# Kernel optimization log

Hardware: AMD Instinct MI355X
Metric: run time of the kernel (lower is better)

The kernel has to match this reference:

```python
import jax, jax.numpy as jnp
import numpy as np

B, C, N, R = 4, 256, 4096, 8
CR = C // R  # 32


def _bn(x, s, b):
    # inference-mode BatchNorm1d folded to per-channel scale/bias; x: [B, C', N]
    return x * s[:, None] + b[:, None]


def setup_inputs() -> dict:
    key = jax.random.key(0)
    ks = jax.random.split(key, 16)
    sc = 1.0 / np.sqrt(C)
    d = {}
    d["x"] = jax.random.normal(ks[0], (B, C, N), jnp.float32)
    d["qk_w"] = jax.random.normal(ks[1], (CR, C), jnp.float32) * sc  # shared q/k 1x1 conv weight
    d["v_w"] = jax.random.normal(ks[2], (C, C), jnp.float32) * sc
    d["v_b"] = jax.random.normal(ks[3], (C,), jnp.float32) * 0.01
    d["trans_w"] = jax.random.normal(ks[4], (C, C), jnp.float32) * sc
    d["trans_b"] = jax.random.normal(ks[5], (C,), jnp.float32) * 0.01
    d["bn1_s"] = 1.0 + 0.1 * jax.random.normal(ks[6], (CR,), jnp.float32)
    d["bn1_b"] = 0.01 * jax.random.normal(ks[7], (CR,), jnp.float32)
    d["bn2_s"] = 1.0 + 0.1 * jax.random.normal(ks[8], (CR,), jnp.float32)
    d["bn2_b"] = 0.01 * jax.random.normal(ks[9], (CR,), jnp.float32)
    d["bn3_s"] = 1.0 + 0.1 * jax.random.normal(ks[10], (C,), jnp.float32)
    d["bn3_b"] = 0.01 * jax.random.normal(ks[11], (C,), jnp.float32)
    d["an_s"] = 1.0 + 0.1 * jax.random.normal(ks[12], (C,), jnp.float32)
    d["an_b"] = 0.01 * jax.random.normal(ks[13], (C,), jnp.float32)
    return d


def reference(x, qk_w, v_w, v_b, trans_w, trans_b,
              bn1_s, bn1_b, bn2_s, bn2_b, bn3_s, bn3_b, an_s, an_b):
    # shared 1x1 conv for q and k (weights tied in the torch module)
    qk = jnp.einsum('oc,bcn->bon', qk_w, x)                       # [B,CR,N]
    x_q = jax.nn.relu(_bn(qk, bn1_s, bn1_b)).transpose(0, 2, 1)   # [B,N,CR]
    x_k = jax.nn.relu(_bn(qk, bn2_s, bn2_b))                      # [B,CR,N]
    x_v = jax.nn.relu(_bn(jnp.einsum('oc,bcn->bon', v_w, x) + v_b[:, None], bn3_s, bn3_b))  # [B,C,N]

    # energy = QK^T + rank-1 correction: -(sum_c q)(sum_c k)^T
    energy = jnp.einsum('bnc,bcm->bnm', x_q, x_k) \
             - x_q.sum(-1)[:, :, None] * x_k.sum(1)[:, None, :]    # [B,N,N]

    att = jax.nn.softmax(energy, axis=-1)
    att = att / (1e-9 + att.sum(axis=1, keepdims=True))            # L1 renorm over dim 1

    x_r = jnp.einsum('bcn,bnm->bcm', x_v, att)                     # [B,C,N]
    diff = x - x_r
    x_r = jax.nn.relu(_bn(jnp.einsum('oc,bcn->bon', trans_w, diff) + trans_b[:, None], an_s, an_b))
    return x + x_r
```

## Files before the change

### kernel.cpp

```cpp
#include <hip/hip_runtime.h>
#include <stdint.h>

#define B_ 4
#define C_ 256
#define N_ 4096
#define L2E 1.4426950408889634f

typedef unsigned short u16;
typedef unsigned int u32;
typedef float f32x4 __attribute__((ext_vector_type(4)));
typedef __bf16 bf16x8 __attribute__((ext_vector_type(8)));

union U16x8 { uint4 q; bf16x8 v; u16 u[8]; __bf16 h[8]; };
union BF2 { u32 w; __bf16 h[2]; };

__device__ __forceinline__ bf16x8 ld_bf8(const u16* p) {
  U16x8 t; t.q = *(const uint4*)p; return t.v;
}
__device__ __forceinline__ f32x4 mfma16(bf16x8 a, bf16x8 b, f32x4 c) {
  return __builtin_amdgcn_mfma_f32_16x16x32_bf16(a, b, c, 0, 0, 0);
}
#define BAR() do { asm volatile("s_waitcnt lgkmcnt(0)" ::: "memory"); \
                   __builtin_amdgcn_s_barrier(); } while (0)


__global__ __launch_bounds__(256) void k_xt(const float* __restrict__ x, u16* __restrict__ xt,
                                            const float* __restrict__ vw, const float* __restrict__ tw,
                                            const float* __restrict__ qkw,
                                            u16* __restrict__ wv, u16* __restrict__ wt, float* __restrict__ wqkt) {
  int bid = blockIdx.x;
  if (bid < 64) {
    int i = bid * 256 + threadIdx.x;
    for (int idx = i; idx < C_ * C_; idx += 16384) {
      BF2 a2, b2; a2.h[0] = (__bf16)vw[idx]; b2.h[0] = (__bf16)tw[idx];
      wv[idx] = (u16)(a2.w & 0xFFFF);
      wt[idx] = (u16)(b2.w & 0xFFFF);
    }
    for (int idx = i; idx < 32 * C_; idx += 16384) {
      int c = idx >> 8, cin = idx & 255;
      wqkt[cin * 32 + c] = qkw[idx];
    }
  }
  int cb = bid & 3, nt = (bid >> 2) & 63, b = bid >> 8;
  __shared__ u16 tile[64][66];
  int t = threadIdx.x, nl = t & 63, cg = t >> 6;
  const float* xp = x + ((size_t)b * C_ + cb * 64) * N_ + nt * 64;
  #pragma unroll
  for (int cc = 0; cc < 16; ++cc) {
    int c = cg * 16 + cc;
    BF2 v; v.h[0] = (__bf16)xp[(size_t)c * N_ + nl];
    tile[c][nl] = (u16)(v.w & 0xFFFF);
  }
  __syncthreads();
  u16* op = xt + ((size_t)b * N_ + nt * 64) * C_ + cb * 64;
  #pragma unroll
  for (int nn = 0; nn < 16; ++nn) {
    int n2 = cg * 16 + nn;
    op[(size_t)n2 * C_ + nl] = tile[nl][n2];
  }
}

__global__ __launch_bounds__(256) void k_qk(
    const float* __restrict__ x, const float* __restrict__ wqkt,
    const float* __restrict__ bn1s, const float* __restrict__ bn1b,
    const float* __restrict__ bn2s, const float* __restrict__ bn2b,
    u16* __restrict__ qfm, u16* __restrict__ kfm,
    float* __restrict__ qsg, float* __restrict__ ksg) {
  int bid = blockIdx.x;
  bid = (bid & 7) * 32 + (bid >> 3);
  int nt = bid & 63, b = bid >> 6;
  int t = threadIdx.x;
  int nl = t & 63;
  int qg = __builtin_amdgcn_readfirstlane(t >> 6);
  int n = nt * 64 + nl;

  __shared__ float red[4][64][33];
  __shared__ float qsum[4][64], ksum[4][64];

  float acc[32];
  #pragma unroll
  for (int c = 0; c < 32; ++c) acc[c] = 0.f;

  const float* xp = x + ((size_t)b * C_ + qg * 64) * N_ + n;
  const float* wp = wqkt + qg * 64 * 32;
  for (int i = 0; i < 64; ++i) {
    float xvv = xp[(size_t)i * N_];
    const float* wr = wp + i * 32;
    #pragma unroll
    for (int c = 0; c < 32; ++c) acc[c] = fmaf(wr[c], xvv, acc[c]);
  }
  #pragma unroll
  for (int c = 0; c < 32; ++c) red[qg][nl][c] = acc[c];
  __syncthreads();

  float pqs = 0.f, pks = 0.f;
  U16x8 tq, tk;
  #pragma unroll
  for (int i2 = 0; i2 < 8; ++i2) {
    int c = qg * 8 + i2;
    float s = red[0][nl][c] + red[1][nl][c] + red[2][nl][c] + red[3][nl][c];
    float fq = fmaxf(fmaf(s, bn1s[c], bn1b[c]), 0.f);
    float fk = fmaxf(fmaf(s, bn2s[c], bn2b[c]), 0.f);
    pqs += fq; pks += fk;
    tq.h[i2] = (__bf16)fq; tk.h[i2] = (__bf16)fk;
  }
  size_t fbase = (((size_t)b * 256 + (n >> 4)) * 64 + (n & 15) + qg * 16) * 8;
  *(uint4*)(qfm + fbase) = tq.q;
  *(uint4*)(kfm + fbase) = tk.q;

  qsum[qg][nl] = pqs; ksum[qg][nl] = pks;
  __syncthreads();
  if (t < 64) {
    int nn2 = nt * 64 + t;
    qsg[b * N_ + nn2] = (qsum[0][t] + qsum[1][t] + qsum[2][t] + qsum[3][t]) * L2E;
    ksg[b * N_ + nn2] = ksum[0][t] + ksum[1][t] + ksum[2][t] + ksum[3][t];
  }
}

template<int MODE>
__global__ __launch_bounds__(256) void k_gemm256(
    const u16* __restrict__ W, const u16* __restrict__ act,
    const float* __restrict__ bias, const float* __restrict__ bns, const float* __restrict__ bnb,
    const float* __restrict__ xres, u16* __restrict__ outb, float* __restrict__ outf) {
  int bid = blockIdx.x;
  bid = (bid & 7) * 64 + (bid >> 3);
  int nt = bid & 127, b = bid >> 7;
  int n0 = nt * 32;
  int t = threadIdx.x;
  int w = t >> 6, l = t & 63, lr = l & 15, lg = l >> 4;

  __shared__ u16 fbuf[16 * 512];

  f32x4 acc[4][2];
  #pragma unroll
  for (int ot = 0; ot < 4; ++ot)
    #pragma unroll
    for (int ns = 0; ns < 2; ++ns) acc[ot][ns] = f32x4{0.f, 0.f, 0.f, 0.f};

  const u16* actp = act + ((size_t)b * N_ + n0) * C_;
  for (int kk = 0; kk < 8; ++kk) {
    int k0 = kk * 32;
    bf16x8 bf[2];
    #pragma unroll
    for (int ns = 0; ns < 2; ++ns)
      bf[ns] = ld_bf8(actp + (size_t)(ns * 16 + lr) * C_ + k0 + lg * 8);
    #pragma unroll
    for (int ot = 0; ot < 4; ++ot) {
      bf16x8 af = ld_bf8(W + (size_t)(w * 64 + ot * 16 + lr) * C_ + k0 + lg * 8);
      #pragma unroll
      for (int ns = 0; ns < 2; ++ns) acc[ot][ns] = mfma16(af, bf[ns], acc[ot][ns]);
    }
  }
  #pragma unroll
  for (int ot = 0; ot < 4; ++ot) {
    #pragma unroll
    for (int r = 0; r < 4; ++r) {
      int oc = w * 64 + ot * 16 + lg * 4 + r;
      float sO = bns[oc], bO = bnb[oc], biO = bias[oc];
      #pragma unroll
      for (int ns = 0; ns < 2; ++ns) {
        float val = fmaxf(fmaf(acc[ot][ns][r] + biO, sO, bO), 0.f);
        if (MODE == 0) {
          int u16off = (lg * 4 + r) * 8 + (lr >> 2) * 128 + ns * 4 + (lr & 3);
          BF2 v; v.h[0] = (__bf16)val;
          fbuf[(w * 4 + ot) * 512 + u16off] = (u16)(v.w & 0xFFFF);
        } else {
          int nn = ns * 16 + lr;
          size_t idx = ((size_t)b * C_ + oc) * N_ + n0 + nn;
          outf[idx] = xres[idx] + val;
        }
      }
    }
  }
  if (MODE == 0) {
    __syncthreads();
    #pragma unroll
    for (int rep = 0; rep < 4; ++rep) {
      int f = rep * 4 + (t >> 6);
      size_t dst = (((size_t)b * 128 + nt) * 16 + f) * 512 + (size_t)(t & 63) * 8;
      *(uint4*)(outb + dst) = *(const uint4*)&fbuf[f * 512 + (t & 63) * 8];
    }
  }
}

__global__ __launch_bounds__(512) void k_phaseA(
    const u16* __restrict__ qfm, const u16* __restrict__ kfm,
    const float* __restrict__ qsg, const float* __restrict__ ksg,
    float* __restrict__ rmg) {
  int bid = blockIdx.x;
  bid = (bid & 7) * 64 + (bid >> 3);
  int nt = bid & 127, b = bid >> 7;
  int bN = b * N_;
  int t = threadIdx.x;
  int w = t >> 6, l = t & 63, lr = l & 15, lg = l >> 4;
  int nsub = w & 1, mq = w >> 1;
  int nrow0 = nt * 32 + nsub * 16;

  __shared__ float pM[4][32], pS[4][32];

  const u16* qf_b = qfm + (size_t)b * 131072;
  const u16* kf_b = kfm + (size_t)b * 131072;

  bf16x8 qf = ld_bf8(qf_b + (size_t)(nrow0 >> 4) * 512 + l * 8);
  f32x4 qsv = *(const f32x4*)(qsg + bN + nrow0 + lg * 4);

  float Mv[4], Sv[4];
  #pragma unroll
  for (int r = 0; r < 4; ++r) { Mv[r] = -3e38f; Sv[r] = 0.f; }

  int mbase = mq * 1024;
  for (int ms = 0; ms < 16; ++ms) {
    float ev[4][4];
    #pragma unroll
    for (int mt2 = 0; mt2 < 4; ++mt2) {
      int m0 = mbase + ms * 64 + mt2 * 16;
      bf16x8 kf = ld_bf8(kf_b + (size_t)(m0 >> 4) * 512 + l * 8);
      f32x4 e = mfma16(qf, kf, f32x4{0.f, 0.f, 0.f, 0.f});
      float ksv = ksg[bN + m0 + lr];
      #pragma unroll
      for (int r = 0; r < 4; ++r) ev[mt2][r] = fmaf(e[r], L2E, -qsv[r] * ksv);
    }
    #pragma unroll
    for (int r = 0; r < 4; ++r) {
      float t0 = fmaxf(fmaxf(ev[0][r], ev[1][r]), fmaxf(ev[2][r], ev[3][r]));
      float Mn = fmaxf(Mv[r], t0);
      Sv[r] = Sv[r] * __builtin_amdgcn_exp2f(Mv[r] - Mn)
            + __builtin_amdgcn_exp2f(ev[0][r] - Mn)
            + __builtin_amdgcn_exp2f(ev[1][r] - Mn)
            + __builtin_amdgcn_exp2f(ev[2][r] - Mn)
            + __builtin_amdgcn_exp2f(ev[3][r] - Mn);
      Mv[r] = Mn;
    }
  }
  #pragma unroll
  for (int off = 1; off < 16; off <<= 1) {
    #pragma unroll
    for (int r = 0; r < 4; ++r) {
      float Mo = __shfl_xor(Mv[r], off);
      float So = __shfl_xor(Sv[r], off);
      float Mn = fmaxf(Mv[r], Mo);
      Sv[r] = Sv[r] * __builtin_amdgcn_exp2f(Mv[r] - Mn)
            + So   * __builtin_amdgcn_exp2f(Mo   - Mn);
      Mv[r] = Mn;
    }
  }
  if (lr == 0) {
    #pragma unroll
    for (int r = 0; r < 4; ++r) {
      pM[mq][nsub * 16 + lg * 4 + r] = Mv[r];
      pS[mq][nsub * 16 + lg * 4 + r] = Sv[r];
    }
  }
  __syncthreads();
  if (t < 32) {
    float M = fmaxf(fmaxf(pM[0][t], pM[1][t]), fmaxf(pM[2][t], pM[3][t]));
    float S = pS[0][t] * __builtin_amdgcn_exp2f(pM[0][t] - M)
            + pS[1][t] * __builtin_amdgcn_exp2f(pM[1][t] - M)
            + pS[2][t] * __builtin_amdgcn_exp2f(pM[2][t] - M)
            + pS[3][t] * __builtin_amdgcn_exp2f(pM[3][t] - M);
    rmg[bN + nt * 32 + t] = M + __builtin_amdgcn_logf(S);
  }
}

__global__ __launch_bounds__(512, 4) void k_phaseB(
    const u16* __restrict__ qfm, const u16* __restrict__ kfm,
    const float* __restrict__ qsg, const float* __restrict__ ksg,
    const float* __restrict__ rmg,
    const u16* __restrict__ vq, const u16* __restrict__ xt,
    u16* __restrict__ diffb) {
  int bid = blockIdx.x;
  bid = (bid & 7) * 64 + (bid >> 3);
  int mt = bid & 127, b = bid >> 7;
  int m0 = mt * 32;
  int bN = b * N_;
  int t = threadIdx.x;
  int w = t >> 6, l = t & 63, lr = l & 15, lg = l >> 4;
  int cq = w & 3, nh = w >> 2;
  int c0 = cq * 64;

  __shared__ __align__(16) char smem[33792];
  u16 (*pbuf)[2][4][1024] = (u16(*)[2][4][1024])smem;
  float (*accl)[2048] = (float(*)[2048])smem;
  float (*csl)[32] = (float(*)[32])(smem + 32768);

  bf16x8 kf0 = ld_bf8(kfm + (size_t)b * 131072 + (size_t)(mt * 2) * 512 + l * 8);
  bf16x8 kf1 = ld_bf8(kfm + (size_t)b * 131072 + (size_t)(mt * 2 + 1) * 512 + l * 8);
  float ks0 = ksg[bN + m0 + lr];
  float ks1 = ksg[bN + m0 + 16 + lr];

  U16x8 onesu;
  #pragma unroll
  for (int i = 0; i < 8; ++i) onesu.u[i] = 0x3F80;
  bf16x8 ones = onesu.v;

  const u16* qf_b = qfm + (size_t)b * 131072;
  const float* qsb = qsg + bN;
  const float* rmb = rmg + bN;
  const u16* vq_b = vq + (size_t)b * 1048576 + (size_t)(cq * 4) * 512 + (size_t)l * 8;

  f32x4 acc0[4], acc1[4];
  #pragma unroll
  for (int ct = 0; ct < 4; ++ct) {
    acc0[ct] = f32x4{0.f, 0.f, 0.f, 0.f};
    acc1[ct] = f32x4{0.f, 0.f, 0.f, 0.f};
  }
  f32x4 accs0 = f32x4{0.f, 0.f, 0.f, 0.f};
  f32x4 accs1 = f32x4{0.f, 0.f, 0.f, 0.f};

  auto produce = [&](int wd, int buf) {
    bf16x8 qf0 = ld_bf8(qf_b + (size_t)(wd * 2) * 512 + l * 8);
    bf16x8 qf1 = ld_bf8(qf_b + (size_t)(wd * 2 + 1) * 512 + l * 8);
    int nb = wd * 32;
    f32x4 qs0 = *(const f32x4*)(qsb + nb + lg * 4);
    f32x4 qs1 = *(const f32x4*)(qsb + nb + 16 + lg * 4);
    f32x4 rm0 = *(const f32x4*)(rmb + nb + lg * 4);
    f32x4 rm1 = *(const f32x4*)(rmb + nb + 16 + lg * 4);

    f32x4 e00 = mfma16(qf0, kf0, f32x4{0.f, 0.f, 0.f, 0.f});
    f32x4 e01 = mfma16(qf1, kf0, f32x4{0.f, 0.f, 0.f, 0.f});
    f32x4 e10 = mfma16(qf0, kf1, f32x4{0.f, 0.f, 0.f, 0.f});
    f32x4 e11 = mfma16(qf1, kf1, f32x4{0.f, 0.f, 0.f, 0.f});

    float p00[4], p01[4], p10[4], p11[4];
    #pragma unroll
    for (int r = 0; r < 4; ++r) {
      p00[r] = __builtin_amdgcn_exp2f(fmaf(qs0[r], -ks0, fmaf(e00[r], L2E, -rm0[r])));
      p01[r] = __builtin_amdgcn_exp2f(fmaf(qs1[r], -ks0, fmaf(e01[r], L2E, -rm1[r])));
      p10[r] = __builtin_amdgcn_exp2f(fmaf(qs0[r], -ks1, fmaf(e10[r], L2E, -rm0[r])));
      p11[r] = __builtin_amdgcn_exp2f(fmaf(qs1[r], -ks1, fmaf(e11[r], L2E, -rm1[r])));
    }
    U16x8 pb0, pb1;
    #pragma unroll
    for (int r = 0; r < 4; ++r) {
      pb0.h[r] = (__bf16)p00[r]; pb0.h[4 + r] = (__bf16)p01[r];
      pb1.h[r] = (__bf16)p10[r]; pb1.h[4 + r] = (__bf16)p11[r];
    }
    accs0 = mfma16(ones, pb0.v, accs0);
    accs1 = mfma16(ones, pb1.v, accs1);
    u16* dst = &pbuf[nh][buf][cq][0];
    *(uint4*)&dst[l * 8] = pb0.q;
    *(uint4*)&dst[512 + l * 8] = pb1.q;
  };

  int wbase = nh * 64;
  produce(wbase + cq, 0);
  BAR();

  for (int g = 0; g < 16; ++g) {
    if (g < 15) produce(wbase + (g + 1) * 4 + cq, (g + 1) & 1);
    int gbuf = g & 1;
    #pragma unroll
    for (int j = 0; j < 4; ++j) {
      int wd = wbase + g * 4 + j;
      const u16* src = &pbuf[nh][gbuf][j][0];
      U16x8 pb0, pb1;
      pb0.q = *(const uint4*)&src[l * 8];
      pb1.q = *(const uint4*)&src[512 + l * 8];
      const u16* vp = vq_b + (size_t)wd * 8192;
      U16x8 v0, v1, v2, v3;
      v0.q = *(const uint4*)(vp);
      v1.q = *(const uint4*)(vp + 512);
      v2.q = *(const uint4*)(vp + 1024);
      v3.q = *(const uint4*)(vp + 1536);
      acc0[0] = mfma16(v0.v, pb0.v, acc0[0]);
      acc1[0] = mfma16(v0.v, pb1.v, acc1[0]);
      acc0[1] = mfma16(v1.v, pb0.v, acc0[1]);
      acc1[1] = mfma16(v1.v, pb1.v, acc1[1]);
      acc0[2] = mfma16(v2.v, pb0.v, acc0[2]);
      acc1[2] = mfma16(v2.v, pb1.v, acc1[2]);
      acc0[3] = mfma16(v3.v, pb0.v, acc0[3]);
      acc1[3] = mfma16(v3.v, pb1.v, acc1[3]);
    }
    BAR();
  }

  if (lg == 0) { csl[w][lr] = accs0[0]; csl[w][16 + lr] = accs1[0]; }
  if (nh == 1) {
    #pragma unroll
    for (int ct = 0; ct < 4; ++ct) {
      *(f32x4*)&accl[cq][(ct * 2 + 0) * 256 + l * 4] = acc0[ct];
      *(f32x4*)&accl[cq][(ct * 2 + 1) * 256 + l * 4] = acc1[ct];
    }
  }
  __syncthreads();
  if (nh == 0) {
    #pragma unroll
    for (int ct = 0; ct < 4; ++ct) {
      acc0[ct] += *(const f32x4*)&accl[cq][(ct * 2 + 0) * 256 + l * 4];
      acc1[ct] += *(const f32x4*)&accl[cq][(ct * 2 + 1) * 256 + l * 4];
    }
    float s0 = 0.f, s1 = 0.f;
    #pragma unroll
    for (int i = 0; i < 8; ++i) { s0 += csl[i][lr]; s1 += csl[i][16 + lr]; }
    float inv0 = __builtin_amdgcn_rcpf(1e-9f + s0);
    float inv1 = __builtin_amdgcn_rcpf(1e-9f + s1);

    #pragma unroll
    for (int ct = 0; ct < 4; ++ct) {
      {
        size_t base = ((size_t)(bN + m0 + lr)) * C_ + c0 + ct * 16 + lg * 4;
        uint2 xv2 = *(const uint2*)(xt + base);
        BF2 xa, xb; xa.w = xv2.x; xb.w = xv2.y;
        BF2 o0, o1;
        o0.h[0] = (__bf16)((float)xa.h[0] - acc0[ct][0] * inv0);
        o0.h[1] = (__bf16)((float)xa.h[1] - acc0[ct][1] * inv0);
        o1.h[0] = (__bf16)((float)xb.h[0] - acc0[ct][2] * inv0);
        o1.h[1] = (__bf16)((float)xb.h[1] - acc0[ct][3] * inv0);
        uint2 ov; ov.x = o0.w; ov.y = o1.w;
        *(uint2*)(diffb + base) = ov;
      }
      {
        size_t base = ((size_t)(bN + m0 + 16 + lr)) * C_ + c0 + ct * 16 + lg * 4;
        uint2 xv2 = *(const uint2*)(xt + base);
        BF2 xa, xb; xa.w = xv2.x; xb.w = xv2.y;
        BF2 o0, o1;
        o0.h[0] = (__bf16)((float)xa.h[0] - acc1[ct][0] * inv1);
        o0.h[1] = (__bf16)((float)xa.h[1] - acc1[ct][1] * inv1);
        o1.h[0] = (__bf16)((float)xb.h[0] - acc1[ct][2] * inv1);
        o1.h[1] = (__bf16)((float)xb.h[1] - acc1[ct][3] * inv1);
        uint2 ov; ov.x = o0.w; ov.y = o1.w;
        *(uint2*)(diffb + base) = ov;
      }
    }
  }
}

extern "C" void kernel_launch(void* const* d_in, const int* in_sizes, int n_in,
                              void* d_out, int out_size, void* d_ws, size_t ws_size,
                              hipStream_t stream) {
  const float* x       = (const float*)d_in[0];
  const float* qk_w    = (const float*)d_in[1];
  const float* v_w     = (const float*)d_in[2];
  const float* v_b     = (const float*)d_in[3];
  const float* trans_w = (const float*)d_in[4];
  const float* trans_b = (const float*)d_in[5];
  const float* bn1s = (const float*)d_in[6];
  const float* bn1b = (const float*)d_in[7];
  const float* bn2s = (const float*)d_in[8];
  const float* bn2b = (const float*)d_in[9];
  const float* bn3s = (const float*)d_in[10];
  const float* bn3b = (const float*)d_in[11];
  const float* ans  = (const float*)d_in[12];
  const float* anb  = (const float*)d_in[13];
  float* out = (float*)d_out;
  char* ws = (char*)d_ws;

  if (ws_size < 27820032) return;

  u16*   xt    = (u16*)(ws + 0);
  u16*   vq    = (u16*)(ws + 8388608);
  u16*   diffb = (u16*)(ws + 16777216);
  u16*   qfm   = (u16*)(ws + 25165824);
  u16*   kfm   = (u16*)(ws + 26214400);
  u16*   wv    = (u16*)(ws + 27262976);
  u16*   wt    = (u16*)(ws + 27394048);
  float* wqkt  = (float*)(ws + 27525120);
  float* qsg   = (float*)(ws + 27557888);
  float* ksg   = (float*)(ws + 27623424);
  float* rmg   = (float*)(ws + 27688960);

  k_xt<<<1024, 256, 0, stream>>>(x, xt, v_w, trans_w, qk_w, wv, wt, wqkt);
  k_qk<<<256, 256, 0, stream>>>(x, wqkt, bn1s, bn1b, bn2s, bn2b, qfm, kfm, qsg, ksg);
  k_gemm256<0><<<512, 256, 0, stream>>>(wv, xt, v_b, bn3s, bn3b, nullptr, vq, nullptr);
  k_phaseA<<<512, 512, 0, stream>>>(qfm, kfm, qsg, ksg, rmg);
  k_phaseB<<<512, 512, 0, stream>>>(qfm, kfm, qsg, ksg, rmg, vq, xt, diffb);
  k_gemm256<1><<<512, 256, 0, stream>>>(wt, diffb, trans_b, ans, anb, x, nullptr, out);
}
```

Baseline: 137.3 us.

## Split phaseB over channel halves, prepack weights into MFMA fragments, stage activations in LDS

The attention-value kernel now launches twice as many blocks. Each block handles half of the channels, so every wave keeps two accumulator tiles instead of four. The goal is more parallelism and lower register pressure, at the price of computing the softmax probabilities twice per query tile. The 1x1-conv weights are pre-swizzled into MFMA fragment order so each wave reads them contiguously. The GEMM stages its activation tile in shared memory, which adds an extra barrier before the output shuffle that reuses that buffer.

```diff
diff --git a/kernel.cpp b/kernel.cpp
--- a/kernel.cpp
+++ b/kernel.cpp
@@ -27,14 +27,16 @@
 __global__ __launch_bounds__(256) void k_xt(const float* __restrict__ x, u16* __restrict__ xt,
                                             const float* __restrict__ vw, const float* __restrict__ tw,
                                             const float* __restrict__ qkw,
-                                            u16* __restrict__ wv, u16* __restrict__ wt, float* __restrict__ wqkt) {
+                                            u16* __restrict__ wvf, u16* __restrict__ wtf, float* __restrict__ wqkt) {
   int bid = blockIdx.x;
   if (bid < 64) {
     int i = bid * 256 + threadIdx.x;
     for (int idx = i; idx < C_ * C_; idx += 16384) {
+      int oc = idx >> 8, c = idx & 255;
+      int dst = (((oc >> 4) * 8 + (c >> 5)) * 64 + (oc & 15) + (((c >> 3) & 3) << 4)) * 8 + (c & 7);
       BF2 a2, b2; a2.h[0] = (__bf16)vw[idx]; b2.h[0] = (__bf16)tw[idx];
-      wv[idx] = (u16)(a2.w & 0xFFFF);
-      wt[idx] = (u16)(b2.w & 0xFFFF);
+      wvf[dst] = (u16)(a2.w & 0xFFFF);
+      wtf[dst] = (u16)(b2.w & 0xFFFF);
     }
     for (int idx = i; idx < 32 * C_; idx += 16384) {
       int c = idx >> 8, cin = idx & 255;
@@ -119,7 +121,7 @@
 
 template<int MODE>
 __global__ __launch_bounds__(256) void k_gemm256(
-    const u16* __restrict__ W, const u16* __restrict__ act,
+    const u16* __restrict__ Wf, const u16* __restrict__ act,
     const float* __restrict__ bias, const float* __restrict__ bns, const float* __restrict__ bnb,
     const float* __restrict__ xres, u16* __restrict__ outb, float* __restrict__ outf) {
   int bid = blockIdx.x;
@@ -129,7 +131,17 @@
   int t = threadIdx.x;
   int w = t >> 6, l = t & 63, lr = l & 15, lg = l >> 4;
 
-  __shared__ u16 fbuf[16 * 512];
+  __shared__ __align__(16) char gsm[32 * 264 * 2];
+  u16 (*atile)[264] = (u16(*)[264])gsm;
+  u16* fbuf = (u16*)gsm;
+
+  const u16* asrc = act + ((size_t)b * N_ + n0) * C_;
+  #pragma unroll
+  for (int rep = 0; rep < 4; ++rep) {
+    int idx8 = rep * 256 + t, row = idx8 >> 5, col8 = idx8 & 31;
+    *(uint4*)&atile[row][col8 * 8] = *(const uint4*)(asrc + (size_t)row * C_ + col8 * 8);
+  }
+  __syncthreads();
 
   f32x4 acc[4][2];
   #pragma unroll
@@ -137,20 +149,20 @@
     #pragma unroll
     for (int ns = 0; ns < 2; ++ns) acc[ot][ns] = f32x4{0.f, 0.f, 0.f, 0.f};
 
-  const u16* actp = act + ((size_t)b * N_ + n0) * C_;
   for (int kk = 0; kk < 8; ++kk) {
-    int k0 = kk * 32;
     bf16x8 bf[2];
     #pragma unroll
     for (int ns = 0; ns < 2; ++ns)
-      bf[ns] = ld_bf8(actp + (size_t)(ns * 16 + lr) * C_ + k0 + lg * 8);
+      bf[ns] = ld_bf8(&atile[ns * 16 + lr][kk * 32 + lg * 8]);
     #pragma unroll
     for (int ot = 0; ot < 4; ++ot) {
-      bf16x8 af = ld_bf8(W + (size_t)(w * 64 + ot * 16 + lr) * C_ + k0 + lg * 8);
+      bf16x8 af = ld_bf8(Wf + (size_t)((w * 4 + ot) * 8 + kk) * 512 + l * 8);
       #pragma unroll
       for (int ns = 0; ns < 2; ++ns) acc[ot][ns] = mfma16(af, bf[ns], acc[ot][ns]);
     }
   }
+  if (MODE == 0) __syncthreads();
+
   #pragma unroll
   for (int ot = 0; ot < 4; ++ot) {
     #pragma unroll
@@ -269,18 +281,20 @@
     const u16* __restrict__ vq, const u16* __restrict__ xt,
     u16* __restrict__ diffb) {
   int bid = blockIdx.x;
-  bid = (bid & 7) * 64 + (bid >> 3);
-  int mt = bid & 127, b = bid >> 7;
+  bid = (bid & 7) * 128 + (bid >> 3);
+  int b = bid >> 8;
+  int ch = (bid >> 7) & 1;
+  int mt = bid & 127;
   int m0 = mt * 32;
   int bN = b * N_;
   int t = threadIdx.x;
   int w = t >> 6, l = t & 63, lr = l & 15, lg = l >> 4;
-  int cq = w & 3, nh = w >> 2;
-  int c0 = cq * 64;
+  int cs = w & 3, nh = w >> 2;
+  int c0 = ch * 128 + cs * 32;
 
   __shared__ __align__(16) char smem[33792];
   u16 (*pbuf)[2][4][1024] = (u16(*)[2][4][1024])smem;
-  float (*accl)[2048] = (float(*)[2048])smem;
+  float (*accl)[1024] = (float(*)[1024])smem;
   float (*csl)[32] = (float(*)[32])(smem + 32768);
 
   bf16x8 kf0 = ld_bf8(kfm + (size_t)b * 131072 + (size_t)(mt * 2) * 512 + l * 8);
@@ -296,11 +310,11 @@
   const u16* qf_b = qfm + (size_t)b * 131072;
   const float* qsb = qsg + bN;
   const float* rmb = rmg + bN;
-  const u16* vq_b = vq + (size_t)b * 1048576 + (size_t)(cq * 4) * 512 + (size_t)l * 8;
-
-  f32x4 acc0[4], acc1[4];
-  #pragma unroll
-  for (int ct = 0; ct < 4; ++ct) {
+  const u16* vq_b = vq + (size_t)b * 1048576 + (size_t)(c0 >> 4) * 512 + (size_t)l * 8;
+
+  f32x4 acc0[2], acc1[2];
+  #pragma unroll
+  for (int ct = 0; ct < 2; ++ct) {
     acc0[ct] = f32x4{0.f, 0.f, 0.f, 0.f};
     acc1[ct] = f32x4{0.f, 0.f, 0.f, 0.f};
   }
@@ -337,17 +351,17 @@
     }
     accs0 = mfma16(ones, pb0.v, accs0);
     accs1 = mfma16(ones, pb1.v, accs1);
-    u16* dst = &pbuf[nh][buf][cq][0];
+    u16* dst = &pbuf[nh][buf][cs][0];
     *(uint4*)&dst[l * 8] = pb0.q;
     *(uint4*)&dst[512 + l * 8] = pb1.q;
   };
 
   int wbase = nh * 64;
-  produce(wbase + cq, 0);
+  produce(wbase + cs, 0);
   BAR();
 
   for (int g = 0; g < 16; ++g) {
-    if (g < 15) produce(wbase + (g + 1) * 4 + cq, (g + 1) & 1);
+    if (g < 15) produce(wbase + (g + 1) * 4 + cs, (g + 1) & 1);
     int gbuf = g & 1;
     #pragma unroll
     for (int j = 0; j < 4; ++j) {
@@ -357,19 +371,13 @@
       pb0.q = *(const uint4*)&src[l * 8];
       pb1.q = *(const uint4*)&src[512 + l * 8];
       const u16* vp = vq_b + (size_t)wd * 8192;
-      U16x8 v0, v1, v2, v3;
+      U16x8 v0, v1;
       v0.q = *(const uint4*)(vp);
       v1.q = *(const uint4*)(vp + 512);
-      v2.q = *(const uint4*)(vp + 1024);
-      v3.q = *(const uint4*)(vp + 1536);
       acc0[0] = mfma16(v0.v, pb0.v, acc0[0]);
       acc1[0] = mfma16(v0.v, pb1.v, acc1[0]);
       acc0[1] = mfma16(v1.v, pb0.v, acc0[1]);
       acc1[1] = mfma16(v1.v, pb1.v, acc1[1]);
-      acc0[2] = mfma16(v2.v, pb0.v, acc0[2]);
-      acc1[2] = mfma16(v2.v, pb1.v, acc1[2]);
-      acc0[3] = mfma16(v3.v, pb0.v, acc0[3]);
-      acc1[3] = mfma16(v3.v, pb1.v, acc1[3]);
     }
     BAR();
   }
@@ -377,17 +385,17 @@
   if (lg == 0) { csl[w][lr] = accs0[0]; csl[w][16 + lr] = accs1[0]; }
   if (nh == 1) {
     #pragma unroll
-    for (int ct = 0; ct < 4; ++ct) {
-      *(f32x4*)&accl[cq][(ct * 2 + 0) * 256 + l * 4] = acc0[ct];
-      *(f32x4*)&accl[cq][(ct * 2 + 1) * 256 + l * 4] = acc1[ct];
+    for (int ct = 0; ct < 2; ++ct) {
+      *(f32x4*)&accl[cs][(ct * 2 + 0) * 256 + l * 4] = acc0[ct];
+      *(f32x4*)&accl[cs][(ct * 2 + 1) * 256 + l * 4] = acc1[ct];
     }
   }
   __syncthreads();
   if (nh == 0) {
     #pragma unroll
-    for (int ct = 0; ct < 4; ++ct) {
-      acc0[ct] += *(const f32x4*)&accl[cq][(ct * 2 + 0) * 256 + l * 4];
-      acc1[ct] += *(const f32x4*)&accl[cq][(ct * 2 + 1) * 256 + l * 4];
+    for (int ct = 0; ct < 2; ++ct) {
+      acc0[ct] += *(const f32x4*)&accl[cs][(ct * 2 + 0) * 256 + l * 4];
+      acc1[ct] += *(const f32x4*)&accl[cs][(ct * 2 + 1) * 256 + l * 4];
     }
     float s0 = 0.f, s1 = 0.f;
     #pragma unroll
@@ -396,7 +404,7 @@
     float inv1 = __builtin_amdgcn_rcpf(1e-9f + s1);
 
     #pragma unroll
-    for (int ct = 0; ct < 4; ++ct) {
+    for (int ct = 0; ct < 2; ++ct) {
       {
         size_t base = ((size_t)(bN + m0 + lr)) * C_ + c0 + ct * 16 + lg * 4;
         uint2 xv2 = *(const uint2*)(xt + base);
@@ -452,17 +460,17 @@
   u16*   diffb = (u16*)(ws + 16777216);
   u16*   qfm   = (u16*)(ws + 25165824);
   u16*   kfm   = (u16*)(ws + 26214400);
-  u16*   wv    = (u16*)(ws + 27262976);
-  u16*   wt    = (u16*)(ws + 27394048);
+  u16*   wvf   = (u16*)(ws + 27262976);
+  u16*   wtf   = (u16*)(ws + 27394048);
   float* wqkt  = (float*)(ws + 27525120);
   float* qsg   = (float*)(ws + 27557888);
   float* ksg   = (float*)(ws + 27623424);
   float* rmg   = (float*)(ws + 27688960);
 
-  k_xt<<<1024, 256, 0, stream>>>(x, xt, v_w, trans_w, qk_w, wv, wt, wqkt);
+  k_xt<<<1024, 256, 0, stream>>>(x, xt, v_w, trans_w, qk_w, wvf, wtf, wqkt);
   k_qk<<<256, 256, 0, stream>>>(x, wqkt, bn1s, bn1b, bn2s, bn2b, qfm, kfm, qsg, ksg);
-  k_gemm256<0><<<512, 256, 0, stream>>>(wv, xt, v_b, bn3s, bn3b, nullptr, vq, nullptr);
+  k_gemm256<0><<<512, 256, 0, stream>>>(wvf, xt, v_b, bn3s, bn3b, nullptr, vq, nullptr);
   k_phaseA<<<512, 512, 0, stream>>>(qfm, kfm, qsg, ksg, rmg);
-  k_phaseB<<<512, 512, 0, stream>>>(qfm, kfm, qsg, ksg, rmg, vq, xt, diffb);
-  k_gemm256<1><<<512, 256, 0, stream>>>(wt, diffb, trans_b, ans, anb, x, nullptr, out);
-}
+  k_phaseB<<<1024, 512, 0, stream>>>(qfm, kfm, qsg, ksg, rmg, vq, xt, diffb);
+  k_gemm256<1><<<512, 256, 0, stream>>>(wtf, diffb, trans_b, ans, anb, x, nullptr, out);
+}
```

New measurement: 128.9 us, median of 4. 6.1% less time.

## Pre-swizzle weights to MFMA fragment layout and stage activations in LDS

Applied to the files above, without the earlier changes.

Weights are written in MFMA fragment order during conversion, so each lane's A-operand load in the 1x1-conv GEMM becomes a contiguous 16-byte read instead of a strided row read. The activation tile for each block is staged once into padded LDS, which is shared by the four waves rather than each wave reloading it from global memory, and the LDS buffer is reused for the output staging. The attention phase B inner MFMA loop also raises wave priority with s_setprio. Costs are an extra barrier and more LDS per block, which may affect occupancy.

```diff
diff --git a/kernel.cpp b/kernel.cpp
--- a/kernel.cpp
+++ b/kernel.cpp
@@ -27,14 +27,16 @@
 __global__ __launch_bounds__(256) void k_xt(const float* __restrict__ x, u16* __restrict__ xt,
                                             const float* __restrict__ vw, const float* __restrict__ tw,
                                             const float* __restrict__ qkw,
-                                            u16* __restrict__ wv, u16* __restrict__ wt, float* __restrict__ wqkt) {
+                                            u16* __restrict__ wvf, u16* __restrict__ wtf, float* __restrict__ wqkt) {
   int bid = blockIdx.x;
   if (bid < 64) {
     int i = bid * 256 + threadIdx.x;
     for (int idx = i; idx < C_ * C_; idx += 16384) {
+      int oc = idx >> 8, c = idx & 255;
+      int dst = (((oc >> 4) * 8 + (c >> 5)) * 64 + (oc & 15) + (((c >> 3) & 3) << 4)) * 8 + (c & 7);
       BF2 a2, b2; a2.h[0] = (__bf16)vw[idx]; b2.h[0] = (__bf16)tw[idx];
-      wv[idx] = (u16)(a2.w & 0xFFFF);
-      wt[idx] = (u16)(b2.w & 0xFFFF);
+      wvf[dst] = (u16)(a2.w & 0xFFFF);
+      wtf[dst] = (u16)(b2.w & 0xFFFF);
     }
     for (int idx = i; idx < 32 * C_; idx += 16384) {
       int c = idx >> 8, cin = idx & 255;
@@ -119,7 +121,7 @@
 
 template<int MODE>
 __global__ __launch_bounds__(256) void k_gemm256(
-    const u16* __restrict__ W, const u16* __restrict__ act,
+    const u16* __restrict__ Wf, const u16* __restrict__ act,
     const float* __restrict__ bias, const float* __restrict__ bns, const float* __restrict__ bnb,
     const float* __restrict__ xres, u16* __restrict__ outb, float* __restrict__ outf) {
   int bid = blockIdx.x;
@@ -129,7 +131,17 @@
   int t = threadIdx.x;
   int w = t >> 6, l = t & 63, lr = l & 15, lg = l >> 4;
 
-  __shared__ u16 fbuf[16 * 512];
+  __shared__ __align__(16) char gsm[32 * 264 * 2];
+  u16 (*atile)[264] = (u16(*)[264])gsm;
+  u16* fbuf = (u16*)gsm;
+
+  const u16* asrc = act + ((size_t)b * N_ + n0) * C_;
+  #pragma unroll
+  for (int rep = 0; rep < 4; ++rep) {
+    int idx8 = rep * 256 + t, row = idx8 >> 5, col8 = idx8 & 31;
+    *(uint4*)&atile[row][col8 * 8] = *(const uint4*)(asrc + (size_t)row * C_ + col8 * 8);
+  }
+  __syncthreads();
 
   f32x4 acc[4][2];
   #pragma unroll
@@ -137,20 +149,20 @@
     #pragma unroll
     for (int ns = 0; ns < 2; ++ns) acc[ot][ns] = f32x4{0.f, 0.f, 0.f, 0.f};
 
-  const u16* actp = act + ((size_t)b * N_ + n0) * C_;
   for (int kk = 0; kk < 8; ++kk) {
-    int k0 = kk * 32;
     bf16x8 bf[2];
     #pragma unroll
     for (int ns = 0; ns < 2; ++ns)
-      bf[ns] = ld_bf8(actp + (size_t)(ns * 16 + lr) * C_ + k0 + lg * 8);
+      bf[ns] = ld_bf8(&atile[ns * 16 + lr][kk * 32 + lg * 8]);
     #pragma unroll
     for (int ot = 0; ot < 4; ++ot) {
-      bf16x8 af = ld_bf8(W + (size_t)(w * 64 + ot * 16 + lr) * C_ + k0 + lg * 8);
+      bf16x8 af = ld_bf8(Wf + (size_t)((w * 4 + ot) * 8 + kk) * 512 + l * 8);
       #pragma unroll
       for (int ns = 0; ns < 2; ++ns) acc[ot][ns] = mfma16(af, bf[ns], acc[ot][ns]);
     }
   }
+  if (MODE == 0) __syncthreads();
+
   #pragma unroll
   for (int ot = 0; ot < 4; ++ot) {
     #pragma unroll
@@ -349,6 +361,7 @@
   for (int g = 0; g < 16; ++g) {
     if (g < 15) produce(wbase + (g + 1) * 4 + cq, (g + 1) & 1);
     int gbuf = g & 1;
+    __builtin_amdgcn_s_setprio(1);
     #pragma unroll
     for (int j = 0; j < 4; ++j) {
       int wd = wbase + g * 4 + j;
@@ -371,6 +384,7 @@
       acc0[3] = mfma16(v3.v, pb0.v, acc0[3]);
       acc1[3] = mfma16(v3.v, pb1.v, acc1[3]);
     }
+    __builtin_amdgcn_s_setprio(0);
     BAR();
   }
 
@@ -452,17 +466,17 @@
   u16*   diffb = (u16*)(ws + 16777216);
   u16*   qfm   = (u16*)(ws + 25165824);
   u16*   kfm   = (u16*)(ws + 26214400);
-  u16*   wv    = (u16*)(ws + 27262976);
-  u16*   wt    = (u16*)(ws + 27394048);
+  u16*   wvf   = (u16*)(ws + 27262976);
+  u16*   wtf   = (u16*)(ws + 27394048);
   float* wqkt  = (float*)(ws + 27525120);
   float* qsg   = (float*)(ws + 27557888);
   float* ksg   = (float*)(ws + 27623424);
   float* rmg   = (float*)(ws + 27688960);
 
-  k_xt<<<1024, 256, 0, stream>>>(x, xt, v_w, trans_w, qk_w, wv, wt, wqkt);
+  k_xt<<<1024, 256, 0, stream>>>(x, xt, v_w, trans_w, qk_w, wvf, wtf, wqkt);
   k_qk<<<256, 256, 0, stream>>>(x, wqkt, bn1s, bn1b, bn2s, bn2b, qfm, kfm, qsg, ksg);
-  k_gemm256<0><<<512, 256, 0, stream>>>(wv, xt, v_b, bn3s, bn3b, nullptr, vq, nullptr);
+  k_gemm256<0><<<512, 256, 0, stream>>>(wvf, xt, v_b, bn3s, bn3b, nullptr, vq, nullptr);
   k_phaseA<<<512, 512, 0, stream>>>(qfm, kfm, qsg, ksg, rmg);
   k_phaseB<<<512, 512, 0, stream>>>(qfm, kfm, qsg, ksg, rmg, vq, xt, diffb);
-  k_gemm256<1><<<512, 256, 0, stream>>>(wt, diffb, trans_b, ans, anb, x, nullptr, out);
-}
+  k_gemm256<1><<<512, 256, 0, stream>>>(wtf, diffb, trans_b, ans, anb, x, nullptr, out);
+}
```

New measurement: 157.1 us. 1.14x slower.
